# Optimization experiments

Hardware: AMD Instinct MI355X
Metric: run time of the kernel (lower is better)

Reference implementation:

```python
import jax, jax.numpy as jnp
import numpy as np
from functools import partial

B, IN, H, OUT, DEPTH = 4096, 1024, 2048, 1024, 8


def setup_inputs() -> dict:
    key = jax.random.key(0)
    ks = jax.random.split(key, 20)
    r = lambda k, shape: jax.random.normal(k, shape, dtype=jnp.float32)
    return {
        "x":  r(ks[0], (B, IN)),
        "W0": r(ks[1], (IN, H)) / np.sqrt(IN),  "b0": r(ks[2], (H,)) * 0.01,
        "W1": r(ks[3], (H, H)) / np.sqrt(H),    "b1": r(ks[4], (H,)) * 0.01,
        "cw1": r(ks[5], (DEPTH, H, H)), "cb1": r(ks[6], (H,)),
        "KW1": r(ks[7], (H, H)) / np.sqrt(H),  "Kb1": r(ks[8], (H,)) * 0.01,
        "W2": r(ks[9], (H, H)) / np.sqrt(H),   "b2": r(ks[10], (H,)) * 0.01,
        "cw2": r(ks[11], (DEPTH, H, H)), "cb2": r(ks[12], (H,)),
        "KW2": r(ks[13], (H, H)) / np.sqrt(H), "Kb2": r(ks[14], (H,)) * 0.01,
        "W3": r(ks[15], (H, OUT)) / np.sqrt(H), "b3": r(ks[16], (OUT,)) * 0.01,
    }


def _cosmic_processing(cw, batch, n_in, n_out):
    # state starts uniform over the n_in-dim 'cosmic' register, one per output j
    s0 = jnp.full((n_out, n_in), 1.0 / np.sqrt(n_in), dtype=cw.dtype)
    angles = cw[:, :, :3]  # (depth, n_out, 3): consciousness/intelligence/wisdom angles

    def step(s, ang):  # s: (n_out, n_in), ang: (n_out, 3)
        # circulant rotation: (M s)[i] = cos*s[i] - sin*s[i+1] + sin*s[i-1]
        for k in range(3):
            c = jnp.cos(ang[:, k])[:, None]
            si = jnp.sin(ang[:, k])[:, None]
            s = c * s - si * jnp.roll(s, -1, axis=1) + si * jnp.roll(s, 1, axis=1)
        return s, None

    s, _ = jax.lax.scan(step, s0, angles)
    prob = jnp.abs(s[:, 0]) ** 2  # (n_out,), sample-independent
    return jnp.broadcast_to(prob[None, :], (batch, n_out))


def _cosmic_layer(x, cw, cb, KW, Kb):
    classical = x @ KW + Kb
    cosmic = _cosmic_processing(cw, x.shape[0], x.shape[1], KW.shape[1])
    return jnp.tanh(classical + cosmic)


def reference(x, W0, b0, W1, b1, cw1, cb1, KW1, Kb1,
              W2, b2, cw2, cb2, KW2, Kb2, W3, b3):
    h = jax.nn.relu(x @ W0 + b0)
    h = jax.nn.relu(h @ W1 + b1)
    h = _cosmic_layer(h, cw1, cb1, KW1, Kb1)
    h = jax.nn.relu(h @ W2 + b2)
    h = _cosmic_layer(h, cw2, cb2, KW2, Kb2)
    return jax.nn.relu(h @ W3 + b3)
```

## Files before the change

### kernel.cpp

```cpp
#include <hip/hip_runtime.h>
#include <math.h>


typedef _Float16 f16;
typedef _Float16 f16x8 __attribute__((ext_vector_type(8)));
typedef _Float16 f16x4 __attribute__((ext_vector_type(4)));
typedef float f32x4 __attribute__((ext_vector_type(4)));

#define GLD16(gp, lp) __builtin_amdgcn_global_load_lds( \
    (const __attribute__((address_space(1))) unsigned int*)(gp), \
    (__attribute__((address_space(3))) unsigned int*)(lp), 16, 0, 0)

__device__ __forceinline__ float tanh_fast(float x) {
  return 1.0f - 2.0f / (__expf(2.0f * x) + 1.0f);
}

__global__ void cast_f32_f16(const float* __restrict__ in, f16* __restrict__ out, int n4) {
  int i = blockIdx.x * 256 + threadIdx.x;
  if (i < n4) {
    float4 v = ((const float4*)in)[i];
    f16x4 o = { (f16)v.x, (f16)v.y, (f16)v.z, (f16)v.w };
    ((f16x4*)out)[i] = o;
  }
}

struct TD { const float* src; f16* dst; int K; int N; };
struct TD6 { TD d[6]; };

__global__ void cast_transpose6(TD6 a) {
  TD d = a.d[blockIdx.z];
  const int bx = blockIdx.x * 64;
  const int by = blockIdx.y * 32;
  if (bx >= d.N || by >= d.K) return;
  __shared__ float tile[32][68];
  const int t = threadIdx.x;
#pragma unroll
  for (int pass = 0; pass < 2; ++pass) {
    int idx = t + pass * 256;
    int row = idx >> 4;
    int c4  = (idx & 15) * 4;
    float4 v = *(const float4*)&d.src[(size_t)(by + row) * d.N + bx + c4];
    *(float4*)&tile[row][c4] = v;
  }
  __syncthreads();
  const int nl = t >> 2;
  const int k8 = (t & 3) * 8;
  f16x8 o;
#pragma unroll
  for (int j = 0; j < 8; ++j) o[j] = (f16)tile[k8 + j][nl];
  *(f16x8*)&d.dst[(size_t)(bx + nl) * d.K + by + k8] = o;
}

__global__ void cosmic_pp2(const float* __restrict__ cw1, const float* __restrict__ cw2,
                           float* __restrict__ pp, int H) {
  int i = blockIdx.x * 256 + threadIdx.x;
  if (i >= 16 * H) return;
  const float* cw = (i < 8 * H) ? cw1 : cw2;
  int j = (i < 8 * H) ? i : i - 8 * H;
  const float* a = cw + (size_t)j * H;
  pp[i] = cosf(a[0]) * cosf(a[1]) * cosf(a[2]);
}
__global__ void cosmic_fin2(const float* __restrict__ pp, float* __restrict__ p1,
                            float* __restrict__ p2, int H) {
  int r = blockIdx.x * 256 + threadIdx.x;
  if (r >= 2 * H) return;
  int rr = (r < H) ? r : r - H;
  const float* base = pp + ((r < H) ? 0 : 8 * H);
  float p = 1.0f;
#pragma unroll
  for (int d = 0; d < 8; ++d) p *= base[d * H + rr];
  float v = p * p / (float)H;
  if (r < H) p1[rr] = v; else p2[rr] = v;
}

template <int EPI, int BM, int BN, int WM, int WN, int MINW>
__global__ __launch_bounds__(512, MINW)
void gemm_f16(const f16* __restrict__ A, const f16* __restrict__ BT,
              const float* __restrict__ bias, const float* __restrict__ prob,
              f16* __restrict__ Ch, float* __restrict__ Cf,
              int M, int N, int K, int GX) {
  constexpr int ASZ = BM * 32;
  constexpr int BSZ = BN * 32;
  constexpr int MR  = BM / WM / 16;
  constexpr int NR  = BN / WN / 16;
  constexpr int RA  = ASZ / 4096;
  constexpr int RB  = BSZ / 4096;
  constexpr int NLD = RA + RB;
  __shared__ f16 lds[3 * (ASZ + BSZ)];
  f16* As = lds;
  f16* Bs = lds + 3 * ASZ;

  const int t = threadIdx.x;

  const int nwg = gridDim.x;
  const int bid = blockIdx.x;
  const int swz = (bid & 7) * (nwg >> 3) + (bid >> 3);
  const int bx = swz % GX;
  const int by = swz / GX;
  const int m0 = by * BM;
  const int n0 = bx * BN;

  auto stage_all = [&](int kt, int buf) {
    const int k0 = kt << 5;
#pragma unroll
    for (int q = 0; q < RA; ++q) {
      int F = q * 4096 + t * 8;
      int r = F >> 5, c = (F >> 3) & 3;
      GLD16(A + (size_t)(m0 + r) * K + k0 + ((c ^ (r & 3)) << 3), As + buf * ASZ + F);
    }
#pragma unroll
    for (int q = 0; q < RB; ++q) {
      int F = q * 4096 + t * 8;
      int r = F >> 5, c = (F >> 3) & 3;
      GLD16(BT + (size_t)(n0 + r) * K + k0 + ((c ^ (r & 3)) << 3), Bs + buf * BSZ + F);
    }
  };

  const int wave = t >> 6, lane = t & 63;
  const int wr = wave / WN, wc = wave % WN;
  const int l16 = lane & 15, kq = lane >> 4;

  f32x4 acc[MR][NR] = {};

  const int nt = K >> 5;
  stage_all(0, 0);
  stage_all(1, 1);
  int cur = 0;
  for (int kt = 0; kt < nt; ++kt) {
    if (kt + 1 < nt) {
      asm volatile("s_waitcnt vmcnt(%0)" :: "i"(NLD) : "memory");
    } else {
      asm volatile("s_waitcnt vmcnt(0)" ::: "memory");
    }
    __builtin_amdgcn_s_barrier();
    if (kt + 2 < nt) {
      int sb = cur + 2; if (sb >= 3) sb -= 3;
      stage_all(kt + 2, sb);
    }

    const f16* Ab = As + cur * ASZ;
    const f16* Bb = Bs + cur * BSZ;
    f16x8 a[MR], b[NR];
#pragma unroll
    for (int mr = 0; mr < MR; ++mr) {
      int row = wr * (MR * 16) + mr * 16 + l16;
      a[mr] = *(const f16x8*)&Ab[row * 32 + ((kq ^ (row & 3)) << 3)];
    }
#pragma unroll
    for (int nr = 0; nr < NR; ++nr) {
      int row = wc * (NR * 16) + nr * 16 + l16;
      b[nr] = *(const f16x8*)&Bb[row * 32 + ((kq ^ (row & 3)) << 3)];
    }
    asm volatile("s_waitcnt lgkmcnt(0)" ::: "memory");
    __builtin_amdgcn_sched_barrier(0);
    __builtin_amdgcn_s_setprio(1);
#pragma unroll
    for (int mr = 0; mr < MR; ++mr)
#pragma unroll
      for (int nr = 0; nr < NR; ++nr)
        acc[mr][nr] = __builtin_amdgcn_mfma_f32_16x16x32_f16(a[mr], b[nr], acc[mr][nr], 0, 0, 0);
    __builtin_amdgcn_s_setprio(0);
    cur = (cur + 1 == 3) ? 0 : cur + 1;
  }

#pragma unroll
  for (int nr = 0; nr < NR; ++nr) {
    const int col = n0 + wc * (NR * 16) + nr * 16 + l16;
    float bn = bias[col];
    if (EPI == 1) bn += prob[col];
#pragma unroll
    for (int mr = 0; mr < MR; ++mr) {
      const int rbase = m0 + wr * (MR * 16) + mr * 16 + kq * 4;
#pragma unroll
      for (int q = 0; q < 4; ++q) {
        float v = acc[mr][nr][q] + bn;
        if (EPI == 1) v = tanh_fast(v);
        else v = fmaxf(v, 0.0f);
        if (EPI == 2) Cf[(size_t)(rbase + q) * N + col] = v;
        else Ch[(size_t)(rbase + q) * N + col] = (f16)v;
      }
    }
  }
}

extern "C" void kernel_launch(void* const* d_in, const int* in_sizes, int n_in,
                              void* d_out, int out_size, void* d_ws, size_t ws_size,
                              hipStream_t stream) {
  const float* x   = (const float*)d_in[0];
  const float* W0  = (const float*)d_in[1];
  const float* b0  = (const float*)d_in[2];
  const float* W1  = (const float*)d_in[3];
  const float* b1  = (const float*)d_in[4];
  const float* cw1 = (const float*)d_in[5];
  const float* KW1 = (const float*)d_in[7];
  const float* Kb1 = (const float*)d_in[8];
  const float* W2  = (const float*)d_in[9];
  const float* b2  = (const float*)d_in[10];
  const float* cw2 = (const float*)d_in[11];
  const float* KW2 = (const float*)d_in[13];
  const float* Kb2 = (const float*)d_in[14];
  const float* W3  = (const float*)d_in[15];
  const float* b3  = (const float*)d_in[16];

  const int B = 4096, IN = 1024, H = 2048, OUT = 1024;

  char* ws = (char*)d_ws;
  size_t off = 0;
  auto alloc = [&](size_t bytes) {
    char* p = ws + off;
    off = (off + bytes + 255) & ~(size_t)255;
    return p;
  };
  f16* xh    = (f16*)alloc((size_t)B * IN * 2);
  f16* W0T   = (f16*)alloc((size_t)H * IN * 2);
  f16* W1T   = (f16*)alloc((size_t)H * H * 2);
  f16* KW1T  = (f16*)alloc((size_t)H * H * 2);
  f16* W2T   = (f16*)alloc((size_t)H * H * 2);
  f16* KW2T  = (f16*)alloc((size_t)H * H * 2);
  f16* W3T   = (f16*)alloc((size_t)OUT * H * 2);
  f16* hA    = (f16*)alloc((size_t)B * H * 2);
  f16* hB    = (f16*)alloc((size_t)B * H * 2);
  float* p1  = (float*)alloc((size_t)H * 4);
  float* p2  = (float*)alloc((size_t)H * 4);
  float* pp  = (float*)alloc((size_t)16 * H * 4);
  (void)ws_size;

  cast_f32_f16<<<(B * IN / 4 + 255) / 256, 256, 0, stream>>>(x, xh, B * IN / 4);

  TD6 td;
  td.d[0] = { W0,  W0T,  IN, H };
  td.d[1] = { W1,  W1T,  H,  H };
  td.d[2] = { KW1, KW1T, H,  H };
  td.d[3] = { W2,  W2T,  H,  H };
  td.d[4] = { KW2, KW2T, H,  H };
  td.d[5] = { W3,  W3T,  H,  OUT };
  cast_transpose6<<<dim3(H / 64, H / 32, 6), 256, 0, stream>>>(td);

  cosmic_pp2<<<(16 * H + 255) / 256, 256, 0, stream>>>(cw1, cw2, pp, H);
  cosmic_fin2<<<(2 * H + 255) / 256, 256, 0, stream>>>(pp, p1, p2, H);

  {
    int gx = H / 128, gy = B / 256;
    dim3 g(gx * gy);
    gemm_f16<0, 256, 128, 4, 2, 4><<<g, 512, 0, stream>>>(xh, W0T, b0,  nullptr, hA, nullptr, B, H, IN, gx);
    gemm_f16<0, 256, 128, 4, 2, 4><<<g, 512, 0, stream>>>(hA, W1T, b1,  nullptr, hB, nullptr, B, H, H,  gx);
    gemm_f16<1, 256, 128, 4, 2, 4><<<g, 512, 0, stream>>>(hB, KW1T, Kb1, p1,     hA, nullptr, B, H, H,  gx);
    gemm_f16<0, 256, 128, 4, 2, 4><<<g, 512, 0, stream>>>(hA, W2T, b2,  nullptr, hB, nullptr, B, H, H,  gx);
    gemm_f16<1, 256, 128, 4, 2, 4><<<g, 512, 0, stream>>>(hB, KW2T, Kb2, p2,     hA, nullptr, B, H, H,  gx);
  }
  {
    int gx = OUT / 128, gy = B / 128;
    dim3 g(gx * gy);
    gemm_f16<2, 128, 128, 2, 4, 2><<<g, 512, 0, stream>>>(hA, W3T, b3, nullptr, nullptr, (float*)d_out, B, OUT, H, gx);
  }
}
```

Before: 249.6 us.

## Restructure GEMM to 256-thread, BK=64 double-buffer with split-K-step LDS loads

```diff
diff --git a/kernel.cpp b/kernel.cpp
--- a/kernel.cpp
+++ b/kernel.cpp
@@ -73,22 +73,22 @@
   if (r < H) p1[rr] = v; else p2[rr] = v;
 }
 
-template <int EPI, int BM, int BN, int WM, int WN, int MINW>
-__global__ __launch_bounds__(512, MINW)
+template <int EPI, int BM, int BN, int MINW>
+__global__ __launch_bounds__(256, MINW)
 void gemm_f16(const f16* __restrict__ A, const f16* __restrict__ BT,
               const float* __restrict__ bias, const float* __restrict__ prob,
               f16* __restrict__ Ch, float* __restrict__ Cf,
               int M, int N, int K, int GX) {
-  constexpr int ASZ = BM * 32;
-  constexpr int BSZ = BN * 32;
-  constexpr int MR  = BM / WM / 16;
-  constexpr int NR  = BN / WN / 16;
-  constexpr int RA  = ASZ / 4096;
-  constexpr int RB  = BSZ / 4096;
+  constexpr int ASZ = BM * 64;
+  constexpr int BSZ = BN * 64;
+  constexpr int MR  = BM / 32;
+  constexpr int NR  = BN / 32;
+  constexpr int RA  = ASZ / 2048;
+  constexpr int RB  = BSZ / 2048;
   constexpr int NLD = RA + RB;
-  __shared__ f16 lds[3 * (ASZ + BSZ)];
+  __shared__ f16 lds[2 * (ASZ + BSZ)];
   f16* As = lds;
-  f16* Bs = lds + 3 * ASZ;
+  f16* Bs = lds + 2 * ASZ;
 
   const int t = threadIdx.x;
 
@@ -101,66 +101,75 @@
   const int n0 = bx * BN;
 
   auto stage_all = [&](int kt, int buf) {
-    const int k0 = kt << 5;
+    const int k0 = kt << 6;
 #pragma unroll
     for (int q = 0; q < RA; ++q) {
-      int F = q * 4096 + t * 8;
-      int r = F >> 5, c = (F >> 3) & 3;
-      GLD16(A + (size_t)(m0 + r) * K + k0 + ((c ^ (r & 3)) << 3), As + buf * ASZ + F);
+      int F = q * 2048 + t * 8;
+      int r = F >> 6, c = (F >> 3) & 7;
+      GLD16(A + (size_t)(m0 + r) * K + k0 + ((c ^ (r & 7)) << 3), As + buf * ASZ + F);
     }
 #pragma unroll
     for (int q = 0; q < RB; ++q) {
-      int F = q * 4096 + t * 8;
-      int r = F >> 5, c = (F >> 3) & 3;
-      GLD16(BT + (size_t)(n0 + r) * K + k0 + ((c ^ (r & 3)) << 3), Bs + buf * BSZ + F);
+      int F = q * 2048 + t * 8;
+      int r = F >> 6, c = (F >> 3) & 7;
+      GLD16(BT + (size_t)(n0 + r) * K + k0 + ((c ^ (r & 7)) << 3), Bs + buf * BSZ + F);
     }
   };
 
   const int wave = t >> 6, lane = t & 63;
-  const int wr = wave / WN, wc = wave % WN;
+  const int wr = wave >> 1, wc = wave & 1;
   const int l16 = lane & 15, kq = lane >> 4;
 
   f32x4 acc[MR][NR] = {};
 
-  const int nt = K >> 5;
+  const int nt = K >> 6;
   stage_all(0, 0);
   stage_all(1, 1);
   int cur = 0;
   for (int kt = 0; kt < nt; ++kt) {
-    if (kt + 1 < nt) {
-      asm volatile("s_waitcnt vmcnt(%0)" :: "i"(NLD) : "memory");
-    } else {
-      asm volatile("s_waitcnt vmcnt(0)" ::: "memory");
-    }
+    if (kt + 1 < nt) asm volatile("s_waitcnt vmcnt(%0)" :: "i"(NLD) : "memory");
+    else             asm volatile("s_waitcnt vmcnt(0)" ::: "memory");
     __builtin_amdgcn_s_barrier();
-    if (kt + 2 < nt) {
-      int sb = cur + 2; if (sb >= 3) sb -= 3;
-      stage_all(kt + 2, sb);
-    }
 
     const f16* Ab = As + cur * ASZ;
     const f16* Bb = Bs + cur * BSZ;
-    f16x8 a[MR], b[NR];
-#pragma unroll
-    for (int mr = 0; mr < MR; ++mr) {
-      int row = wr * (MR * 16) + mr * 16 + l16;
-      a[mr] = *(const f16x8*)&Ab[row * 32 + ((kq ^ (row & 3)) << 3)];
-    }
-#pragma unroll
-    for (int nr = 0; nr < NR; ++nr) {
-      int row = wc * (NR * 16) + nr * 16 + l16;
-      b[nr] = *(const f16x8*)&Bb[row * 32 + ((kq ^ (row & 3)) << 3)];
-    }
+    f16x8 a[2][MR], b[2][NR];
+#pragma unroll
+    for (int s = 0; s < 2; ++s) {
+      const int cc = s * 4 + kq;
+#pragma unroll
+      for (int mr = 0; mr < MR; ++mr) {
+        int row = wr * (MR * 16) + mr * 16 + l16;
+        a[s][mr] = *(const f16x8*)&Ab[row * 64 + ((cc ^ (row & 7)) << 3)];
+      }
+#pragma unroll
+      for (int nr = 0; nr < NR; ++nr) {
+        int row = wc * (NR * 16) + nr * 16 + l16;
+        b[s][nr] = *(const f16x8*)&Bb[row * 64 + ((cc ^ (row & 7)) << 3)];
+      }
+      __builtin_amdgcn_sched_barrier(0);
+    }
+    asm volatile("s_waitcnt lgkmcnt(%0)" :: "i"(MR + NR) : "memory");
+    __builtin_amdgcn_sched_barrier(0);
+    __builtin_amdgcn_s_setprio(1);
+#pragma unroll
+    for (int mr = 0; mr < MR; ++mr)
+#pragma unroll
+      for (int nr = 0; nr < NR; ++nr)
+        acc[mr][nr] = __builtin_amdgcn_mfma_f32_16x16x32_f16(a[0][mr], b[0][nr], acc[mr][nr], 0, 0, 0);
+    __builtin_amdgcn_s_setprio(0);
     asm volatile("s_waitcnt lgkmcnt(0)" ::: "memory");
     __builtin_amdgcn_sched_barrier(0);
+    __builtin_amdgcn_s_barrier();
+    if (kt + 2 < nt) stage_all(kt + 2, cur);
     __builtin_amdgcn_s_setprio(1);
 #pragma unroll
     for (int mr = 0; mr < MR; ++mr)
 #pragma unroll
       for (int nr = 0; nr < NR; ++nr)
-        acc[mr][nr] = __builtin_amdgcn_mfma_f32_16x16x32_f16(a[mr], b[nr], acc[mr][nr], 0, 0, 0);
+        acc[mr][nr] = __builtin_amdgcn_mfma_f32_16x16x32_f16(a[1][mr], b[1][nr], acc[mr][nr], 0, 0, 0);
     __builtin_amdgcn_s_setprio(0);
-    cur = (cur + 1 == 3) ? 0 : cur + 1;
+    cur ^= 1;
   }
 
 #pragma unroll
@@ -240,17 +249,17 @@
   cosmic_fin2<<<(2 * H + 255) / 256, 256, 0, stream>>>(pp, p1, p2, H);
 
   {
-    int gx = H / 128, gy = B / 256;
+    int gx = H / 128, gy = B / 128;
     dim3 g(gx * gy);
-    gemm_f16<0, 256, 128, 4, 2, 4><<<g, 512, 0, stream>>>(xh, W0T, b0,  nullptr, hA, nullptr, B, H, IN, gx);
-    gemm_f16<0, 256, 128, 4, 2, 4><<<g, 512, 0, stream>>>(hA, W1T, b1,  nullptr, hB, nullptr, B, H, H,  gx);
-    gemm_f16<1, 256, 128, 4, 2, 4><<<g, 512, 0, stream>>>(hB, KW1T, Kb1, p1,     hA, nullptr, B, H, H,  gx);
-    gemm_f16<0, 256, 128, 4, 2, 4><<<g, 512, 0, stream>>>(hA, W2T, b2,  nullptr, hB, nullptr, B, H, H,  gx);
-    gemm_f16<1, 256, 128, 4, 2, 4><<<g, 512, 0, stream>>>(hB, KW2T, Kb2, p2,     hA, nullptr, B, H, H,  gx);
+    gemm_f16<0, 128, 128, 2><<<g, 256, 0, stream>>>(xh, W0T, b0,  nullptr, hA, nullptr, B, H, IN, gx);
+    gemm_f16<0, 128, 128, 2><<<g, 256, 0, stream>>>(hA, W1T, b1,  nullptr, hB, nullptr, B, H, H,  gx);
+    gemm_f16<1, 128, 128, 2><<<g, 256, 0, stream>>>(hB, KW1T, Kb1, p1,     hA, nullptr, B, H, H,  gx);
+    gemm_f16<0, 128, 128, 2><<<g, 256, 0, stream>>>(hA, W2T, b2,  nullptr, hB, nullptr, B, H, H,  gx);
+    gemm_f16<1, 128, 128, 2><<<g, 256, 0, stream>>>(hB, KW2T, Kb2, p2,     hA, nullptr, B, H, H,  gx);
   }
   {
-    int gx = OUT / 128, gy = B / 128;
+    int gx = OUT / 64, gy = B / 128;
     dim3 g(gx * gy);
-    gemm_f16<2, 128, 128, 2, 4, 2><<<g, 512, 0, stream>>>(hA, W3T, b3, nullptr, nullptr, (float*)d_out, B, OUT, H, gx);
-  }
-}
+    gemm_f16<2, 128, 64, 3><<<g, 256, 0, stream>>>(hA, W3T, b3, nullptr, nullptr, (float*)d_out, B, OUT, H, gx);
+  }
+}
```

New measurement: 211.9 us. 15.1% less time.
